# Performance work log

Hardware: AMD Instinct MI355X
Metric: run time of the kernel (lower is better)

Reference implementation:

```python
import jax, jax.numpy as jnp
import numpy as np

DIM = 32
N_ENTITY = 500000
N_RELATION = 64
N_USER = 100000
N_ITEM = 200000
B = 4096
K = 64
L = 2


def setup_inputs() -> dict:
    key = jax.random.key(0)
    ks = jax.random.split(key, 14)
    users = jax.random.randint(ks[0], (B,), 0, N_USER)
    items = jax.random.randint(ks[1], (B,), 0, N_ITEM)
    hop0_items = jax.random.randint(ks[2], (B, K), 0, N_ENTITY)
    heads = jax.random.randint(ks[3], (L, B, K), 0, N_ENTITY)
    relations = jax.random.randint(ks[4], (L, B, K), 0, N_RELATION)
    tails = jax.random.randint(ks[5], (L, B, K), 0, N_ENTITY)
    # xavier-uniform-style embedding tables
    def xavier(k, shape):
        bound = float(np.sqrt(6.0 / (shape[0] + shape[1])))
        return jax.random.uniform(k, shape, jnp.float32, -bound, bound)
    entity_emb = xavier(ks[6], (N_ENTITY, DIM))
    relation_emb = xavier(ks[7], (N_RELATION, DIM))
    rec_user_emb = xavier(ks[8], (N_USER, DIM))
    rec_item_emb = xavier(ks[9], (N_ITEM, DIM))
    # RNN params (torch default init: U(-1/sqrt(hidden), 1/sqrt(hidden)))
    b = 1.0 / float(np.sqrt(DIM))
    W_ih = jax.random.uniform(ks[10], (DIM, 2 * DIM), jnp.float32, -b, b)
    W_hh = jax.random.uniform(ks[11], (DIM, DIM), jnp.float32, -b, b)
    b_ih = jax.random.uniform(ks[12], (DIM,), jnp.float32, -b, b)
    b_hh = jax.random.uniform(ks[13], (DIM,), jnp.float32, -b, b)
    return {
        "users": users, "items": items, "hop0_items": hop0_items,
        "heads": heads, "relations": relations, "tails": tails,
        "entity_emb": entity_emb, "relation_emb": relation_emb,
        "rec_user_emb": rec_user_emb, "rec_item_emb": rec_item_emb,
        "W_ih": W_ih, "W_hh": W_hh, "b_ih": b_ih, "b_hh": b_hh,
    }


def reference(users, items, hop0_items, heads, relations, tails,
              entity_emb, relation_emb, rec_user_emb, rec_item_emb,
              W_ih, W_hh, b_ih, b_hh):
    # hop-0: sum of item embeddings in each user's seed set  [B, dim]
    o = entity_emb[hop0_items].sum(axis=1)
    n_hops = heads.shape[0]
    for l in range(n_hops):
        h = entity_emb[heads[l]]        # [B, K, d]
        r = relation_emb[relations[l]]  # [B, K, d]
        tl = entity_emb[tails[l]]       # [B, K, d]
        hr = jnp.concatenate([h, r], axis=-1)   # [B, K, 2d]
        tr = jnp.concatenate([tl, r], axis=-1)  # [B, K, 2d]
        # attention over the K triples of each user
        pi = jax.nn.softmax((hr * tr).sum(axis=-1), axis=1)[..., None]  # [B,K,1]
        # 2-step tanh RNN over sequence (hr, tr), h0 = 0; take final hidden state
        h1 = jnp.tanh(jnp.einsum('bke,de->bkd', hr, W_ih) + b_ih + b_hh)
        h2 = jnp.tanh(jnp.einsum('bke,de->bkd', tr, W_ih)
                      + jnp.einsum('bkd,ed->bke', h1, W_hh) + b_ih + b_hh)
        o = o + (pi * h2).sum(axis=1)
    user_embeddings = o + rec_user_emb[users]
    item_embeddings = entity_emb[items] + rec_item_emb[items]
    return jax.nn.sigmoid((user_embeddings * item_embeddings).sum(axis=1))
```

## Files before the change

kernel.cpp:

```cpp
#include <hip/hip_runtime.h>

#define DIM 32
#define KK 64
#define NHOP 2
#define WPB 4
#define XPAD 80
#define WLDS (64 * XPAD + 256)

typedef __attribute__((ext_vector_type(8)))  short bf16x8;
typedef __attribute__((ext_vector_type(16))) float f32x16;
typedef __attribute__((ext_vector_type(4)))  unsigned int u32x4;

__device__ __forceinline__ float rcp_fast(float x) { return __builtin_amdgcn_rcpf(x); }

__device__ __forceinline__ float tanh_fast(float x) {
    float t = __expf(2.0f * x);
    return 1.0f - 2.0f * rcp_fast(t + 1.0f);
}

__device__ __forceinline__ unsigned pk2(float lo, float hi) {
    return __builtin_amdgcn_perm(__builtin_bit_cast(unsigned, hi),
                                 __builtin_bit_cast(unsigned, lo), 0x07060302u);
}

__device__ __forceinline__ bf16x8 frag_ld(const unsigned char* Xb, int row, int oct) {
    u32x4 v = *(const u32x4*)(Xb + row * XPAD + oct * 16);
    return __builtin_bit_cast(bf16x8, v);
}

__device__ __forceinline__ void pack_row(const float4* v, u32x4* u) {
    #pragma unroll
    for (int i = 0; i < 4; ++i) {
        u[i][0] = pk2(v[2*i].x,   v[2*i].y);
        u[i][1] = pk2(v[2*i].z,   v[2*i].w);
        u[i][2] = pk2(v[2*i+1].x, v[2*i+1].y);
        u[i][3] = pk2(v[2*i+1].z, v[2*i+1].w);
    }
}

__global__ __launch_bounds__(256) void ripple_mfma(
    const int* __restrict__ users,
    const int* __restrict__ items,
    const int* __restrict__ hop0_items,
    const int* __restrict__ heads,
    const int* __restrict__ relations,
    const int* __restrict__ tails,
    const float* __restrict__ entity_emb,
    const float* __restrict__ relation_emb,
    const float* __restrict__ rec_user_emb,
    const float* __restrict__ rec_item_emb,
    const float* __restrict__ W_ih,
    const float* __restrict__ W_hh,
    const float* __restrict__ b_ih,
    const float* __restrict__ b_hh,
    float* __restrict__ out,
    const int B)
{
    __shared__ __align__(16) unsigned char smem[WPB * WLDS];
    const int wave = threadIdx.x >> 6;
    const int lane = threadIdx.x & 63;
    const int h5   = lane >> 5;
    const int p    = lane & 31;

    unsigned char* Xb = smem + wave * WLDS;
    float* qb = (float*)(Xb + 64 * XPAD);
    float* bb = qb + 32;

    const int b = __builtin_amdgcn_readfirstlane(blockIdx.x * WPB + wave);
    if (b >= B) return;

    const int it = __builtin_amdgcn_readfirstlane(items[b]);
    const int uu = __builtin_amdgcn_readfirstlane(users[b]);

    float tpart = 0.0f;

    if (lane < DIM) {
        float qd = entity_emb[(size_t)it * DIM + lane] + rec_item_emb[(size_t)it * DIM + lane];
        qb[lane] = qd;
        tpart += rec_user_emb[(size_t)uu * DIM + lane] * qd;
    } else {
        int d = lane - DIM;
        bb[d] = b_ih[d] + b_hh[d];
    }

    bf16x8 wih[4], whh[2];
    {
        const float* wr = W_ih + p * (2 * DIM);
        #pragma unroll
        for (int kt = 0; kt < 4; ++kt) {
            const float* s = wr + kt * 16 + h5 * 8;
            u32x4 u;
            #pragma unroll
            for (int j = 0; j < 4; ++j) u[j] = pk2(s[2*j], s[2*j+1]);
            wih[kt] = __builtin_bit_cast(bf16x8, u);
        }
        const float* wr2 = W_hh + p * DIM;
        #pragma unroll
        for (int kt = 0; kt < 2; ++kt) {
            const float* s = wr2 + kt * 16 + h5 * 8;
            u32x4 u;
            #pragma unroll
            for (int j = 0; j < 4; ++j) u[j] = pk2(s[2*j], s[2*j+1]);
            whh[kt] = __builtin_bit_cast(bf16x8, u);
        }
    }

    {
        const int idx = hop0_items[b * KK + lane];
        const float4* rp = (const float4*)(entity_emb + (size_t)idx * DIM);
        const float4* qp = (const float4*)qb;
        float part = 0.0f;
        #pragma unroll
        for (int i = 0; i < 8; ++i) {
            float4 v = rp[i]; float4 qv = qp[i];
            part = fmaf(v.x, qv.x, part);
            part = fmaf(v.y, qv.y, part);
            part = fmaf(v.z, qv.z, part);
            part = fmaf(v.w, qv.w, part);
        }
        tpart += part;
    }

    u32x4* Xrow = (u32x4*)(Xb + lane * XPAD);

    #pragma unroll 1
    for (int l = 0; l < NHOP; ++l) {
        const int base = (l * B + b) * KK + lane;
        const int ih  = heads[base];
        const int ir  = relations[base];
        const int itv = tails[base];

        float4 hv[8], tv[8];
        {
            const float4* hp = (const float4*)(entity_emb + (size_t)ih  * DIM);
            const float4* tp = (const float4*)(entity_emb + (size_t)itv * DIM);
            #pragma unroll
            for (int i = 0; i < 8; ++i) hv[i] = hp[i];
            #pragma unroll
            for (int i = 0; i < 8; ++i) tv[i] = tp[i];
        }
        float score = 0.0f;
        #pragma unroll
        for (int i = 0; i < 8; ++i) {
            score = fmaf(hv[i].x, tv[i].x, score);
            score = fmaf(hv[i].y, tv[i].y, score);
            score = fmaf(hv[i].z, tv[i].z, score);
            score = fmaf(hv[i].w, tv[i].w, score);
        }
        u32x4 hu[4], tu[4];
        pack_row(hv, hu);
        pack_row(tv, tu);

        u32x4 ru[4];
        {
            float4 rv[8];
            const float4* rp = (const float4*)(relation_emb + (size_t)ir * DIM);
            #pragma unroll
            for (int i = 0; i < 8; ++i) rv[i] = rp[i];
            #pragma unroll
            for (int i = 0; i < 8; ++i) {
                score = fmaf(rv[i].x, rv[i].x, score);
                score = fmaf(rv[i].y, rv[i].y, score);
                score = fmaf(rv[i].z, rv[i].z, score);
                score = fmaf(rv[i].w, rv[i].w, score);
            }
            pack_row(rv, ru);
        }

        #pragma unroll
        for (int i = 0; i < 4; ++i) Xrow[i] = ru[i];

        f32x16 accA[2], accB[2];
        {
            f32x16 bias_v;
            const float4* bp = (const float4*)bb;
            #pragma unroll
            for (int Q = 0; Q < 4; ++Q) {
                float4 bq = bp[2 * Q + h5];
                bias_v[4*Q+0] = bq.x; bias_v[4*Q+1] = bq.y;
                bias_v[4*Q+2] = bq.z; bias_v[4*Q+3] = bq.w;
            }
            accA[0] = bias_v; accA[1] = bias_v;
        }
        #pragma unroll
        for (int nt = 0; nt < 2; ++nt)
            #pragma unroll
            for (int kt = 0; kt < 2; ++kt)
                accA[nt] = __builtin_amdgcn_mfma_f32_32x32x16_bf16(
                    wih[2 + kt], frag_ld(Xb, 32*nt + p, 2*kt + h5), accA[nt], 0, 0, 0);
        accB[0] = accA[0]; accB[1] = accA[1];

        #pragma unroll
        for (int i = 0; i < 4; ++i) Xrow[i] = hu[i];
        #pragma unroll
        for (int nt = 0; nt < 2; ++nt)
            #pragma unroll
            for (int kt = 0; kt < 2; ++kt)
                accB[nt] = __builtin_amdgcn_mfma_f32_32x32x16_bf16(
                    wih[kt], frag_ld(Xb, 32*nt + p, 2*kt + h5), accB[nt], 0, 0, 0);

        #pragma unroll
        for (int i = 0; i < 4; ++i) Xrow[i] = tu[i];
        #pragma unroll
        for (int nt = 0; nt < 2; ++nt)
            #pragma unroll
            for (int kt = 0; kt < 2; ++kt)
                accA[nt] = __builtin_amdgcn_mfma_f32_32x32x16_bf16(
                    wih[kt], frag_ld(Xb, 32*nt + p, 2*kt + h5), accA[nt], 0, 0, 0);

        #pragma unroll
        for (int nt = 0; nt < 2; ++nt) {
            float t0[16];
            #pragma unroll
            for (int j = 0; j < 16; ++j) t0[j] = tanh_fast(accB[nt][j]);
            unsigned char* hrow = Xb + (32 * nt + p) * XPAD;
            #pragma unroll
            for (int Q = 0; Q < 4; ++Q) {
                uint2 w;
                w.x = pk2(t0[4*Q+0], t0[4*Q+1]);
                w.y = pk2(t0[4*Q+2], t0[4*Q+3]);
                *(uint2*)(hrow + 16 * Q + 8 * h5) = w;
            }
        }

        #pragma unroll
        for (int nt = 0; nt < 2; ++nt)
            #pragma unroll
            for (int kt = 0; kt < 2; ++kt)
                accA[nt] = __builtin_amdgcn_mfma_f32_32x32x16_bf16(
                    whh[kt], frag_ld(Xb, 32*nt + p, 2*kt + h5), accA[nt], 0, 0, 0);

        float qf[16];
        {
            const float4* qp4 = (const float4*)qb;
            #pragma unroll
            for (int Q = 0; Q < 4; ++Q) {
                float4 v = qp4[2 * Q + h5];
                qf[4*Q+0] = v.x; qf[4*Q+1] = v.y; qf[4*Q+2] = v.z; qf[4*Q+3] = v.w;
            }
        }
        float sd0 = 0.0f, sd1 = 0.0f;
        #pragma unroll
        for (int j = 0; j < 16; ++j) sd0 = fmaf(tanh_fast(accA[0][j]), qf[j], sd0);
        #pragma unroll
        for (int j = 0; j < 16; ++j) sd1 = fmaf(tanh_fast(accA[1][j]), qf[j], sd1);
        sd0 += __shfl_xor(sd0, 32, 64);
        sd1 += __shfl_xor(sd1, 32, 64);
        float sown = (lane < 32) ? sd0 : sd1;

        float ex  = __expf(score);
        float num = ex * sown, den = ex;
        #pragma unroll
        for (int m = 1; m <= 32; m <<= 1) {
            num += __shfl_xor(num, m, 64);
            den += __shfl_xor(den, m, 64);
        }
        tpart += (lane == 0) ? num * rcp_fast(den) : 0.0f;
    }

    #pragma unroll
    for (int m = 1; m <= 32; m <<= 1) tpart += __shfl_xor(tpart, m, 64);
    if (lane == 0) out[b] = rcp_fast(1.0f + __expf(-tpart));
}

extern "C" void kernel_launch(void* const* d_in, const int* in_sizes, int n_in,
                              void* d_out, int out_size, void* d_ws, size_t ws_size,
                              hipStream_t stream)
{
    const int* users = (const int*)d_in[0];
    const int* items = (const int*)d_in[1];
    const int* hop0  = (const int*)d_in[2];
    const int* heads = (const int*)d_in[3];
    const int* rels  = (const int*)d_in[4];
    const int* tails = (const int*)d_in[5];
    const float* entity_emb   = (const float*)d_in[6];
    const float* relation_emb = (const float*)d_in[7];
    const float* rec_user_emb = (const float*)d_in[8];
    const float* rec_item_emb = (const float*)d_in[9];
    const float* W_ih = (const float*)d_in[10];
    const float* W_hh = (const float*)d_in[11];
    const float* b_ih = (const float*)d_in[12];
    const float* b_hh = (const float*)d_in[13];
    float* out = (float*)d_out;

    const int B = in_sizes[0];
    const int blocks = (B + WPB - 1) / WPB;
    hipLaunchKernelGGL(ripple_mfma, dim3(blocks), dim3(256), 0, stream,
                       users, items, hop0, rels ? heads : heads, rels, tails,
                       entity_emb, relation_emb, rec_user_emb, rec_item_emb,
                       W_ih, W_hh, b_ih, b_hh, out, B);
}
```

Baseline: 48.90 us.

## Split work per hop across waves and load MFMA fragments directly from registers

The single per-user wave is split into three independent waves (hop-0/user term, hop 1, hop 2), each writing a partial score to workspace, and a second small kernel sums the partials and applies the sigmoid. Gathered head/tail/relation rows are loaded straight into MFMA B-fragment layout, so the LDS staging of X is skipped. Weights are packed once per block into LDS instead of per wave. This adds parallelism and memory-level concurrency, at the cost of an extra kernel launch, a workspace round trip, and redundant reloads of the query embedding.

```diff
diff --git a/kernel.cpp b/kernel.cpp
--- a/kernel.cpp
+++ b/kernel.cpp
@@ -2,14 +2,17 @@
 
 #define DIM 32
 #define KK 64
-#define NHOP 2
 #define WPB 4
-#define XPAD 80
-#define WLDS (64 * XPAD + 256)
-
-typedef __attribute__((ext_vector_type(8)))  short bf16x8;
-typedef __attribute__((ext_vector_type(16))) float f32x16;
-typedef __attribute__((ext_vector_type(4)))  unsigned int u32x4;
+#define WIH_STRIDE 144
+#define WHH_STRIDE 80
+#define H1_STRIDE 80
+#define LDS_WIH (32 * WIH_STRIDE)
+#define LDS_WHH (32 * WHH_STRIDE)
+#define LDS_H1  (KK * H1_STRIDE)
+
+typedef short bf16x8 __attribute__((ext_vector_type(8)));
+typedef float f32x16 __attribute__((ext_vector_type(16)));
+typedef unsigned int u32x4 __attribute__((ext_vector_type(4)));
 
 __device__ __forceinline__ float rcp_fast(float x) { return __builtin_amdgcn_rcpf(x); }
 
@@ -23,22 +26,20 @@
                                  __builtin_bit_cast(unsigned, lo), 0x07060302u);
 }
 
-__device__ __forceinline__ bf16x8 frag_ld(const unsigned char* Xb, int row, int oct) {
-    u32x4 v = *(const u32x4*)(Xb + row * XPAD + oct * 16);
-    return __builtin_bit_cast(bf16x8, v);
-}
-
-__device__ __forceinline__ void pack_row(const float4* v, u32x4* u) {
-    #pragma unroll
-    for (int i = 0; i < 4; ++i) {
-        u[i][0] = pk2(v[2*i].x,   v[2*i].y);
-        u[i][1] = pk2(v[2*i].z,   v[2*i].w);
-        u[i][2] = pk2(v[2*i+1].x, v[2*i+1].y);
-        u[i][3] = pk2(v[2*i+1].z, v[2*i+1].w);
-    }
-}
-
-__global__ __launch_bounds__(256) void ripple_mfma(
+__device__ __forceinline__ bf16x8 pack8(float4 a, float4 b) {
+    u32x4 u;
+    u[0] = pk2(a.x, a.y); u[1] = pk2(a.z, a.w);
+    u[2] = pk2(b.x, b.y); u[3] = pk2(b.z, b.w);
+    return __builtin_bit_cast(bf16x8, u);
+}
+
+__device__ __forceinline__ float dot4(float4 a, float4 b) {
+    float s = a.x * b.x;
+    s = fmaf(a.y, b.y, s); s = fmaf(a.z, b.z, s); s = fmaf(a.w, b.w, s);
+    return s;
+}
+
+__global__ __launch_bounds__(256) void ripple_k1(
     const int* __restrict__ users,
     const int* __restrict__ items,
     const int* __restrict__ hop0_items,
@@ -53,214 +54,237 @@
     const float* __restrict__ W_hh,
     const float* __restrict__ b_ih,
     const float* __restrict__ b_hh,
-    float* __restrict__ out,
+    float* __restrict__ ws,
     const int B)
 {
-    __shared__ __align__(16) unsigned char smem[WPB * WLDS];
-    const int wave = threadIdx.x >> 6;
-    const int lane = threadIdx.x & 63;
+    __shared__ __align__(16) unsigned char lds[LDS_WIH + LDS_WHH + WPB * LDS_H1];
+    unsigned char* wihL = lds;
+    unsigned char* whhL = lds + LDS_WIH;
+    unsigned char* h1L  = lds + LDS_WIH + LDS_WHH;
+
+    const int tid = threadIdx.x;
+
+    #pragma unroll
+    for (int c = 0; c < 4; ++c) {
+        int i = tid + 256 * c;
+        int row = i >> 5, dw = i & 31;
+        *(unsigned*)(wihL + row * WIH_STRIDE + dw * 4) =
+            pk2(W_ih[row * 64 + 2 * dw], W_ih[row * 64 + 2 * dw + 1]);
+    }
+    #pragma unroll
+    for (int c = 0; c < 2; ++c) {
+        int i = tid + 256 * c;
+        int row = i >> 4, dw = i & 15;
+        *(unsigned*)(whhL + row * WHH_STRIDE + dw * 4) =
+            pk2(W_hh[row * 32 + 2 * dw], W_hh[row * 32 + 2 * dw + 1]);
+    }
+    __syncthreads();
+
+    const int wv   = tid >> 6;
+    const int lane = tid & 63;
     const int h5   = lane >> 5;
     const int p    = lane & 31;
-
-    unsigned char* Xb = smem + wave * WLDS;
-    float* qb = (float*)(Xb + 64 * XPAD);
-    float* bb = qb + 32;
-
-    const int b = __builtin_amdgcn_readfirstlane(blockIdx.x * WPB + wave);
-    if (b >= B) return;
-
-    const int it = __builtin_amdgcn_readfirstlane(items[b]);
-    const int uu = __builtin_amdgcn_readfirstlane(users[b]);
-
-    float tpart = 0.0f;
-
-    if (lane < DIM) {
-        float qd = entity_emb[(size_t)it * DIM + lane] + rec_item_emb[(size_t)it * DIM + lane];
-        qb[lane] = qd;
-        tpart += rec_user_emb[(size_t)uu * DIM + lane] * qd;
-    } else {
-        int d = lane - DIM;
-        bb[d] = b_ih[d] + b_hh[d];
-    }
-
-    bf16x8 wih[4], whh[2];
-    {
-        const float* wr = W_ih + p * (2 * DIM);
-        #pragma unroll
-        for (int kt = 0; kt < 4; ++kt) {
-            const float* s = wr + kt * 16 + h5 * 8;
-            u32x4 u;
-            #pragma unroll
-            for (int j = 0; j < 4; ++j) u[j] = pk2(s[2*j], s[2*j+1]);
-            wih[kt] = __builtin_bit_cast(bf16x8, u);
-        }
-        const float* wr2 = W_hh + p * DIM;
-        #pragma unroll
-        for (int kt = 0; kt < 2; ++kt) {
-            const float* s = wr2 + kt * 16 + h5 * 8;
-            u32x4 u;
-            #pragma unroll
-            for (int j = 0; j < 4; ++j) u[j] = pk2(s[2*j], s[2*j+1]);
-            whh[kt] = __builtin_bit_cast(bf16x8, u);
-        }
-    }
-
-    {
+    const int w    = blockIdx.x * WPB + wv;
+    if (w >= 3 * B) return;
+
+    int role, b0;
+    if (w < B)          { role = 0; b0 = w; }
+    else if (w < 2 * B) { role = 1; b0 = w - B; }
+    else                { role = 2; b0 = w - 2 * B; }
+    const int b = __builtin_amdgcn_readfirstlane(b0);
+
+    if (role == 0) {
+        const int it = __builtin_amdgcn_readfirstlane(items[b]);
+        const int uu = __builtin_amdgcn_readfirstlane(users[b]);
+        float q[DIM];
+        #pragma unroll
+        for (int d = 0; d < DIM; ++d)
+            q[d] = entity_emb[(size_t)it * DIM + d] + rec_item_emb[(size_t)it * DIM + d];
+        float up = 0.0f;
+        #pragma unroll
+        for (int d = 0; d < DIM; ++d)
+            up = fmaf(rec_user_emb[(size_t)uu * DIM + d], q[d], up);
+
         const int idx = hop0_items[b * KK + lane];
         const float4* rp = (const float4*)(entity_emb + (size_t)idx * DIM);
-        const float4* qp = (const float4*)qb;
         float part = 0.0f;
         #pragma unroll
         for (int i = 0; i < 8; ++i) {
-            float4 v = rp[i]; float4 qv = qp[i];
-            part = fmaf(v.x, qv.x, part);
-            part = fmaf(v.y, qv.y, part);
-            part = fmaf(v.z, qv.z, part);
-            part = fmaf(v.w, qv.w, part);
+            float4 v = rp[i];
+            part = fmaf(v.x, q[4*i+0], part);
+            part = fmaf(v.y, q[4*i+1], part);
+            part = fmaf(v.z, q[4*i+2], part);
+            part = fmaf(v.w, q[4*i+3], part);
         }
-        tpart += part;
-    }
-
-    u32x4* Xrow = (u32x4*)(Xb + lane * XPAD);
-
-    #pragma unroll 1
-    for (int l = 0; l < NHOP; ++l) {
-        const int base = (l * B + b) * KK + lane;
-        const int ih  = heads[base];
-        const int ir  = relations[base];
-        const int itv = tails[base];
-
-        float4 hv[8], tv[8];
-        {
-            const float4* hp = (const float4*)(entity_emb + (size_t)ih  * DIM);
-            const float4* tp = (const float4*)(entity_emb + (size_t)itv * DIM);
-            #pragma unroll
-            for (int i = 0; i < 8; ++i) hv[i] = hp[i];
-            #pragma unroll
-            for (int i = 0; i < 8; ++i) tv[i] = tp[i];
+        #pragma unroll
+        for (int m = 1; m <= 32; m <<= 1) part += __shfl_xor(part, m, 64);
+        if (lane == 0) ws[b] = part + up;
+        return;
+    }
+
+    const int l = role - 1;
+    const int base = (l * B + b) * KK;
+
+    const int iAh = heads[base + p],       iBh = heads[base + 32 + p];
+    const int iAr = relations[base + p],   iBr = relations[base + 32 + p];
+    const int iAt = tails[base + p],       iBt = tails[base + 32 + p];
+
+    float4 gh[8], gt[8], gr[8];
+    {
+        const float* a = entity_emb + (size_t)iAh * DIM + 8 * h5;
+        const float* bb_ = entity_emb + (size_t)iBh * DIM + 8 * h5;
+        gh[0] = *(const float4*)(a);      gh[1] = *(const float4*)(a + 4);
+        gh[2] = *(const float4*)(a + 16); gh[3] = *(const float4*)(a + 20);
+        gh[4] = *(const float4*)(bb_);      gh[5] = *(const float4*)(bb_ + 4);
+        gh[6] = *(const float4*)(bb_ + 16); gh[7] = *(const float4*)(bb_ + 20);
+    }
+    {
+        const float* a = entity_emb + (size_t)iAt * DIM + 8 * h5;
+        const float* bb_ = entity_emb + (size_t)iBt * DIM + 8 * h5;
+        gt[0] = *(const float4*)(a);      gt[1] = *(const float4*)(a + 4);
+        gt[2] = *(const float4*)(a + 16); gt[3] = *(const float4*)(a + 20);
+        gt[4] = *(const float4*)(bb_);      gt[5] = *(const float4*)(bb_ + 4);
+        gt[6] = *(const float4*)(bb_ + 16); gt[7] = *(const float4*)(bb_ + 20);
+    }
+    {
+        const float* a = relation_emb + (size_t)iAr * DIM + 8 * h5;
+        const float* bb_ = relation_emb + (size_t)iBr * DIM + 8 * h5;
+        gr[0] = *(const float4*)(a);      gr[1] = *(const float4*)(a + 4);
+        gr[2] = *(const float4*)(a + 16); gr[3] = *(const float4*)(a + 20);
+        gr[4] = *(const float4*)(bb_);      gr[5] = *(const float4*)(bb_ + 4);
+        gr[6] = *(const float4*)(bb_ + 16); gr[7] = *(const float4*)(bb_ + 20);
+    }
+
+    const int it = __builtin_amdgcn_readfirstlane(items[b]);
+    float qf[16], bv[16];
+    #pragma unroll
+    for (int Q = 0; Q < 4; ++Q) {
+        const int d0 = 8 * Q + 4 * h5;
+        float4 qe = *(const float4*)(entity_emb   + (size_t)it * DIM + d0);
+        float4 qr = *(const float4*)(rec_item_emb + (size_t)it * DIM + d0);
+        float4 bi = *(const float4*)(b_ih + d0);
+        float4 bh = *(const float4*)(b_hh + d0);
+        qf[4*Q+0] = qe.x + qr.x; qf[4*Q+1] = qe.y + qr.y;
+        qf[4*Q+2] = qe.z + qr.z; qf[4*Q+3] = qe.w + qr.w;
+        bv[4*Q+0] = bi.x + bh.x; bv[4*Q+1] = bi.y + bh.y;
+        bv[4*Q+2] = bi.z + bh.z; bv[4*Q+3] = bi.w + bh.w;
+    }
+
+    float scA = 0.0f, scB = 0.0f;
+    #pragma unroll
+    for (int i = 0; i < 4; ++i) {
+        scA += dot4(gh[i], gt[i]);
+        scA += dot4(gr[i], gr[i]);
+    }
+    #pragma unroll
+    for (int i = 4; i < 8; ++i) {
+        scB += dot4(gh[i], gt[i]);
+        scB += dot4(gr[i], gr[i]);
+    }
+
+    bf16x8 hf[2][2], tf[2][2], rf[2][2];
+    #pragma unroll
+    for (int nt = 0; nt < 2; ++nt)
+        #pragma unroll
+        for (int kt = 0; kt < 2; ++kt) {
+            hf[nt][kt] = pack8(gh[nt*4 + kt*2], gh[nt*4 + kt*2 + 1]);
+            tf[nt][kt] = pack8(gt[nt*4 + kt*2], gt[nt*4 + kt*2 + 1]);
+            rf[nt][kt] = pack8(gr[nt*4 + kt*2], gr[nt*4 + kt*2 + 1]);
         }
-        float score = 0.0f;
-        #pragma unroll
-        for (int i = 0; i < 8; ++i) {
-            score = fmaf(hv[i].x, tv[i].x, score);
-            score = fmaf(hv[i].y, tv[i].y, score);
-            score = fmaf(hv[i].z, tv[i].z, score);
-            score = fmaf(hv[i].w, tv[i].w, score);
+
+    bf16x8 wihF[4], whhF[2];
+    #pragma unroll
+    for (int kt = 0; kt < 4; ++kt)
+        wihF[kt] = __builtin_bit_cast(bf16x8,
+            *(const u32x4*)(wihL + p * WIH_STRIDE + kt * 32 + h5 * 16));
+    #pragma unroll
+    for (int kt = 0; kt < 2; ++kt)
+        whhF[kt] = __builtin_bit_cast(bf16x8,
+            *(const u32x4*)(whhL + p * WHH_STRIDE + kt * 32 + h5 * 16));
+
+    f32x16 accA[2], accB[2];
+    {
+        f32x16 bias_v;
+        #pragma unroll
+        for (int j = 0; j < 16; ++j) bias_v[j] = bv[j];
+        accA[0] = bias_v; accA[1] = bias_v;
+    }
+    #pragma unroll
+    for (int nt = 0; nt < 2; ++nt)
+        #pragma unroll
+        for (int kt = 0; kt < 2; ++kt)
+            accA[nt] = __builtin_amdgcn_mfma_f32_32x32x16_bf16(
+                wihF[2 + kt], rf[nt][kt], accA[nt], 0, 0, 0);
+    accB[0] = accA[0]; accB[1] = accA[1];
+    #pragma unroll
+    for (int nt = 0; nt < 2; ++nt)
+        #pragma unroll
+        for (int kt = 0; kt < 2; ++kt)
+            accB[nt] = __builtin_amdgcn_mfma_f32_32x32x16_bf16(
+                wihF[kt], hf[nt][kt], accB[nt], 0, 0, 0);
+    #pragma unroll
+    for (int nt = 0; nt < 2; ++nt)
+        #pragma unroll
+        for (int kt = 0; kt < 2; ++kt)
+            accA[nt] = __builtin_amdgcn_mfma_f32_32x32x16_bf16(
+                wihF[kt], tf[nt][kt], accA[nt], 0, 0, 0);
+
+    unsigned char* myh1 = h1L + wv * LDS_H1;
+    #pragma unroll
+    for (int nt = 0; nt < 2; ++nt) {
+        float t0[16];
+        #pragma unroll
+        for (int j = 0; j < 16; ++j) t0[j] = tanh_fast(accB[nt][j]);
+        unsigned char* hrow = myh1 + (32 * nt + p) * H1_STRIDE;
+        #pragma unroll
+        for (int Q = 0; Q < 4; ++Q) {
+            uint2 wq;
+            wq.x = pk2(t0[4*Q+0], t0[4*Q+1]);
+            wq.y = pk2(t0[4*Q+2], t0[4*Q+3]);
+            *(uint2*)(hrow + 16 * Q + 8 * h5) = wq;
         }
-        u32x4 hu[4], tu[4];
-        pack_row(hv, hu);
-        pack_row(tv, tu);
-
-        u32x4 ru[4];
-        {
-            float4 rv[8];
-            const float4* rp = (const float4*)(relation_emb + (size_t)ir * DIM);
-            #pragma unroll
-            for (int i = 0; i < 8; ++i) rv[i] = rp[i];
-            #pragma unroll
-            for (int i = 0; i < 8; ++i) {
-                score = fmaf(rv[i].x, rv[i].x, score);
-                score = fmaf(rv[i].y, rv[i].y, score);
-                score = fmaf(rv[i].z, rv[i].z, score);
-                score = fmaf(rv[i].w, rv[i].w, score);
-            }
-            pack_row(rv, ru);
+    }
+    #pragma unroll
+    for (int nt = 0; nt < 2; ++nt)
+        #pragma unroll
+        for (int kt = 0; kt < 2; ++kt) {
+            bf16x8 h1f = __builtin_bit_cast(bf16x8,
+                *(const u32x4*)(myh1 + (32 * nt + p) * H1_STRIDE + (2 * kt + h5) * 16));
+            accA[nt] = __builtin_amdgcn_mfma_f32_32x32x16_bf16(
+                whhF[kt], h1f, accA[nt], 0, 0, 0);
         }
 
-        #pragma unroll
-        for (int i = 0; i < 4; ++i) Xrow[i] = ru[i];
-
-        f32x16 accA[2], accB[2];
-        {
-            f32x16 bias_v;
-            const float4* bp = (const float4*)bb;
-            #pragma unroll
-            for (int Q = 0; Q < 4; ++Q) {
-                float4 bq = bp[2 * Q + h5];
-                bias_v[4*Q+0] = bq.x; bias_v[4*Q+1] = bq.y;
-                bias_v[4*Q+2] = bq.z; bias_v[4*Q+3] = bq.w;
-            }
-            accA[0] = bias_v; accA[1] = bias_v;
-        }
-        #pragma unroll
-        for (int nt = 0; nt < 2; ++nt)
-            #pragma unroll
-            for (int kt = 0; kt < 2; ++kt)
-                accA[nt] = __builtin_amdgcn_mfma_f32_32x32x16_bf16(
-                    wih[2 + kt], frag_ld(Xb, 32*nt + p, 2*kt + h5), accA[nt], 0, 0, 0);
-        accB[0] = accA[0]; accB[1] = accA[1];
-
-        #pragma unroll
-        for (int i = 0; i < 4; ++i) Xrow[i] = hu[i];
-        #pragma unroll
-        for (int nt = 0; nt < 2; ++nt)
-            #pragma unroll
-            for (int kt = 0; kt < 2; ++kt)
-                accB[nt] = __builtin_amdgcn_mfma_f32_32x32x16_bf16(
-                    wih[kt], frag_ld(Xb, 32*nt + p, 2*kt + h5), accB[nt], 0, 0, 0);
-
-        #pragma unroll
-        for (int i = 0; i < 4; ++i) Xrow[i] = tu[i];
-        #pragma unroll
-        for (int nt = 0; nt < 2; ++nt)
-            #pragma unroll
-            for (int kt = 0; kt < 2; ++kt)
-                accA[nt] = __builtin_amdgcn_mfma_f32_32x32x16_bf16(
-                    wih[kt], frag_ld(Xb, 32*nt + p, 2*kt + h5), accA[nt], 0, 0, 0);
-
-        #pragma unroll
-        for (int nt = 0; nt < 2; ++nt) {
-            float t0[16];
-            #pragma unroll
-            for (int j = 0; j < 16; ++j) t0[j] = tanh_fast(accB[nt][j]);
-            unsigned char* hrow = Xb + (32 * nt + p) * XPAD;
-            #pragma unroll
-            for (int Q = 0; Q < 4; ++Q) {
-                uint2 w;
-                w.x = pk2(t0[4*Q+0], t0[4*Q+1]);
-                w.y = pk2(t0[4*Q+2], t0[4*Q+3]);
-                *(uint2*)(hrow + 16 * Q + 8 * h5) = w;
-            }
-        }
-
-        #pragma unroll
-        for (int nt = 0; nt < 2; ++nt)
-            #pragma unroll
-            for (int kt = 0; kt < 2; ++kt)
-                accA[nt] = __builtin_amdgcn_mfma_f32_32x32x16_bf16(
-                    whh[kt], frag_ld(Xb, 32*nt + p, 2*kt + h5), accA[nt], 0, 0, 0);
-
-        float qf[16];
-        {
-            const float4* qp4 = (const float4*)qb;
-            #pragma unroll
-            for (int Q = 0; Q < 4; ++Q) {
-                float4 v = qp4[2 * Q + h5];
-                qf[4*Q+0] = v.x; qf[4*Q+1] = v.y; qf[4*Q+2] = v.z; qf[4*Q+3] = v.w;
-            }
-        }
-        float sd0 = 0.0f, sd1 = 0.0f;
-        #pragma unroll
-        for (int j = 0; j < 16; ++j) sd0 = fmaf(tanh_fast(accA[0][j]), qf[j], sd0);
-        #pragma unroll
-        for (int j = 0; j < 16; ++j) sd1 = fmaf(tanh_fast(accA[1][j]), qf[j], sd1);
-        sd0 += __shfl_xor(sd0, 32, 64);
-        sd1 += __shfl_xor(sd1, 32, 64);
-        float sown = (lane < 32) ? sd0 : sd1;
-
-        float ex  = __expf(score);
-        float num = ex * sown, den = ex;
-        #pragma unroll
-        for (int m = 1; m <= 32; m <<= 1) {
-            num += __shfl_xor(num, m, 64);
-            den += __shfl_xor(den, m, 64);
-        }
-        tpart += (lane == 0) ? num * rcp_fast(den) : 0.0f;
-    }
-
-    #pragma unroll
-    for (int m = 1; m <= 32; m <<= 1) tpart += __shfl_xor(tpart, m, 64);
-    if (lane == 0) out[b] = rcp_fast(1.0f + __expf(-tpart));
+    scA += __shfl_xor(scA, 32, 64);
+    scB += __shfl_xor(scB, 32, 64);
+    const float e0 = __expf(scA);
+    const float e1 = __expf(scB);
+
+    float sd0 = 0.0f, sd1 = 0.0f;
+    #pragma unroll
+    for (int j = 0; j < 16; ++j) sd0 = fmaf(tanh_fast(accA[0][j]), qf[j], sd0);
+    #pragma unroll
+    for (int j = 0; j < 16; ++j) sd1 = fmaf(tanh_fast(accA[1][j]), qf[j], sd1);
+    sd0 += __shfl_xor(sd0, 32, 64);
+    sd1 += __shfl_xor(sd1, 32, 64);
+
+    float num = e0 * sd0 + e1 * sd1;
+    float den = e0 + e1;
+    #pragma unroll
+    for (int m = 1; m <= 16; m <<= 1) {
+        num += __shfl_xor(num, m, 64);
+        den += __shfl_xor(den, m, 64);
+    }
+    if (lane == 0) ws[(1 + l) * B + b] = num * rcp_fast(den);
+}
+
+__global__ __launch_bounds__(256) void ripple_k2(
+    const float* __restrict__ ws, float* __restrict__ out, const int B)
+{
+    const int i = blockIdx.x * 256 + threadIdx.x;
+    if (i < B) {
+        const float s = ws[i] + ws[B + i] + ws[2 * B + i];
+        out[i] = rcp_fast(1.0f + __expf(-s));
+    }
 }
 
 extern "C" void kernel_launch(void* const* d_in, const int* in_sizes, int n_in,
@@ -282,11 +306,15 @@
     const float* b_ih = (const float*)d_in[12];
     const float* b_hh = (const float*)d_in[13];
     float* out = (float*)d_out;
+    float* ws  = (float*)d_ws;
 
     const int B = in_sizes[0];
-    const int blocks = (B + WPB - 1) / WPB;
-    hipLaunchKernelGGL(ripple_mfma, dim3(blocks), dim3(256), 0, stream,
-                       users, items, hop0, rels ? heads : heads, rels, tails,
+    const int blocks1 = (3 * B + WPB - 1) / WPB;
+    hipLaunchKernelGGL(ripple_k1, dim3(blocks1), dim3(256), 0, stream,
+                       users, items, hop0, heads, rels, tails,
                        entity_emb, relation_emb, rec_user_emb, rec_item_emb,
-                       W_ih, W_hh, b_ih, b_hh, out, B);
-}
+                       W_ih, W_hh, b_ih, b_hh, ws, B);
+    const int blocks2 = (B + 255) / 256;
+    hipLaunchKernelGGL(ripple_k2, dim3(blocks2), dim3(256), 0, stream,
+                       ws, out, B);
+}
```

Result: no change. 49.84 us (+1.9%).
